# Kernel tuning notes

Hardware: AMD Instinct MI355X
Metric: run time of the kernel (lower is better)

## Reference

```python
import jax, jax.numpy as jnp
import numpy as np
import math

B, H, W = 2, 64, 64
D_MODEL = 192
D_STATE = 16
EXPAND = 1
D_INNER = EXPAND * D_MODEL
DT_RANK = math.ceil(D_MODEL / 16)  # 'auto' -> 12
DT_MIN, DT_MAX, DT_FLOOR = 0.001, 0.1, 0.0001


def setup_inputs() -> dict:
    key = jax.random.key(0)
    ks = jax.random.split(key, 10)
    x = jax.random.normal(ks[0], (B, H, W, D_MODEL), jnp.float32)
    in_proj_w = jax.random.normal(ks[1], (D_INNER, D_MODEL), jnp.float32) * (D_MODEL ** -0.5)
    in_proj_b = jnp.zeros((D_INNER,), jnp.float32)
    x_proj_w = jax.random.normal(ks[2], (2 * DT_RANK + 3 * D_STATE, D_INNER), jnp.float32) * (D_INNER ** -0.5)
    dt_init_std = DT_RANK ** -0.5
    dt_projT_w = jax.random.uniform(ks[3], (D_INNER, DT_RANK), jnp.float32, -dt_init_std, dt_init_std)
    dt_projL_w = jax.random.uniform(ks[4], (D_INNER, DT_RANK), jnp.float32, -dt_init_std, dt_init_std)
    # dt bias init: inverse-softplus of dt sampled log-uniform in [dt_min, dt_max]
    dt = jnp.exp(jax.random.uniform(ks[5], (D_INNER,), jnp.float32) * (math.log(DT_MAX) - math.log(DT_MIN)) + math.log(DT_MIN))
    dt = jnp.clip(dt, DT_FLOOR, None)
    inv_dt = dt + jnp.log(-jnp.expm1(-dt))
    dt_projT_b = inv_dt
    dt_projL_b = inv_dt
    A_init = jnp.tile(jnp.arange(1, D_STATE + 1, dtype=jnp.float32), (D_INNER, 1))  # [D_INNER, N]
    AT_log = jnp.log(A_init)
    AL_log = jnp.log(A_init)
    D_skip = jnp.ones((D_INNER,), jnp.float32)
    out_proj_w = jax.random.normal(ks[6], (D_MODEL, D_INNER), jnp.float32) * (D_INNER ** -0.5)
    out_proj_b = jnp.zeros((D_MODEL,), jnp.float32)
    return {"x": x, "in_proj_w": in_proj_w, "in_proj_b": in_proj_b, "x_proj_w": x_proj_w,
            "dt_projT_w": dt_projT_w, "dt_projT_b": dt_projT_b, "dt_projL_w": dt_projL_w,
            "dt_projL_b": dt_projL_b, "AT_log": AT_log, "AL_log": AL_log, "D_skip": D_skip,
            "out_proj_w": out_proj_w, "out_proj_b": out_proj_b}


def _wavefront_ssm(u, x_proj_w, dt_projT_w, dt_projT_b, dt_projL_w, dt_projL_b, AT_log, AL_log, D_skip):
    # u: [B,H,W,D_INNER]. 2D selective scan: state at (i,j) mixes top (i-1,j) and left (i,j-1).
    R, N = DT_RANK, D_STATE
    proj = jnp.einsum('bhwd,pd->bhwp', u, x_proj_w)  # [B,H,W,2R+3N]
    dtT_r = proj[..., :R]
    dtL_r = proj[..., R:2 * R]
    B_T = proj[..., 2 * R:2 * R + N]            # [B,H,W,N]
    B_L = proj[..., 2 * R + N:2 * R + 2 * N]    # [B,H,W,N]
    C = proj[..., 2 * R + 2 * N:]               # [B,H,W,N]
    deltaT = jax.nn.softplus(jnp.einsum('bhwr,dr->bhwd', dtT_r, dt_projT_w) + dt_projT_b)  # [B,H,W,D]
    deltaL = jax.nn.softplus(jnp.einsum('bhwr,dr->bhwd', dtL_r, dt_projL_w) + dt_projL_b)
    AT = -jnp.exp(AT_log)  # [D,N]
    AL = -jnp.exp(AL_log)
    dAT = jnp.exp(deltaT[..., None] * AT)  # [B,H,W,D,N]
    dAL = jnp.exp(deltaL[..., None] * AL)
    dB = (deltaT[..., None] * B_T[..., None, :] + deltaL[..., None] * B_L[..., None, :]) * u[..., None]  # [B,H,W,D,N]
    # reorder to [H,W,B,D,N] for scanning
    dAT_s = jnp.transpose(dAT, (1, 2, 0, 3, 4))
    dAL_s = jnp.transpose(dAL, (1, 2, 0, 3, 4))
    dB_s = jnp.transpose(dB, (1, 2, 0, 3, 4))

    def row_step(h_prev_row, row):  # h_prev_row: [W,B,D,N]
        dAT_r, dAL_r, dB_r = row
        top = dAT_r * h_prev_row + dB_r  # top-neighbor contribution + input, per column

        def col_step(h_left, cols):  # h_left: [B,D,N]
            t, a = cols
            h = t + a * h_left
            return h, h

        h0 = jnp.zeros_like(h_prev_row[0])
        _, h_row = jax.lax.scan(col_step, h0, (top, dAL_r))  # [W,B,D,N]
        return h_row, h_row

    h_init = jnp.zeros((W, u.shape[0], D_INNER, N), u.dtype)
    _, hs = jax.lax.scan(row_step, h_init, (dAT_s, dAL_s, dB_s))  # [H,W,B,D,N]
    h = jnp.transpose(hs, (2, 0, 1, 3, 4))  # [B,H,W,D,N]
    y = jnp.einsum('bhwdn,bhwn->bhwd', h, C) + u * D_skip
    return y


def reference(x, in_proj_w, in_proj_b, x_proj_w, dt_projT_w, dt_projT_b,
              dt_projL_w, dt_projL_b, AT_log, AL_log, D_skip, out_proj_w, out_proj_b):
    u = jax.nn.gelu(jnp.einsum('bhwc,dc->bhwd', x, in_proj_w) + in_proj_b, approximate=False)
    y = _wavefront_ssm(u, x_proj_w, dt_projT_w, dt_projT_b, dt_projL_w, dt_projL_b, AT_log, AL_log, D_skip)
    y = jax.nn.gelu(y, approximate=False)
    out = jnp.einsum('bhwd,cd->bhwc', y, out_proj_w) + out_proj_b
    return out
```

## Files before the change

### kernel.cpp

```cpp
#include <hip/hip_runtime.h>
#include <math.h>

#define DM 192
#define RNK 12
#define NS 16
#define NO2 432

#define OFF_FLAG   156672u
#define OFF_PY0    156688u
#define OFF_PY1    1729552u
#define OFF_YG     3302416u
#define OFF_DIAG   5268496u
#define OFF_TL2    6841360u
#define OFF_BC4D   9987088u

typedef __attribute__((ext_vector_type(8))) short short8v;
typedef __attribute__((ext_vector_type(4))) float floatx4;

__device__ __forceinline__ float gelu_f(float x){
    return 0.5f * x * (1.0f + erff(x * 0.70710678118654752f));
}
__device__ __forceinline__ float softplus_f(float x){
    return fmaxf(x, 0.0f) + log1pf(__expf(-fabsf(x)));
}
__device__ __forceinline__ int diag_off(int s){
    return (s <= 64) ? ((s * (s + 1)) >> 1) : (2080 + (((s - 64) * (191 - s)) >> 1));
}
__device__ __forceinline__ void inv_diag(int q, int& i_out, int& j_out){
    int s;
    if (q < 2080){
        s = (int)((sqrtf(8.0f * (float)q + 1.0f) - 1.0f) * 0.5f);
        while (((s + 1) * (s + 2)) / 2 <= q) s++;
        while ((s * (s + 1)) / 2 > q) s--;
    } else {
        const int q2 = 4095 - q;
        int t = (int)((sqrtf(8.0f * (float)q2 + 1.0f) - 1.0f) * 0.5f);
        while (((t + 1) * (t + 2)) / 2 <= q2) t++;
        while ((t * (t + 1)) / 2 > q2) t--;
        s = 126 - t;
    }
    const int jmin = (s > 63) ? (s - 63) : 0;
    const int j = jmin + (q - diag_off(s));
    j_out = j;
    i_out = s - j;
}
__device__ __forceinline__ unsigned short bf16_rte(float f){
    unsigned u = __float_as_uint(f);
    unsigned r = (u + 0x7fffu + ((u >> 16) & 1u)) >> 16;
    return (unsigned short)r;
}
__device__ __forceinline__ float bf16_f(unsigned short h){
    return __uint_as_float(((unsigned)h) << 16);
}
__device__ __forceinline__ void split8(float4 v0, float4 v1, short8v& hi, short8v& lo){
    float f[8] = {v0.x, v0.y, v0.z, v0.w, v1.x, v1.y, v1.z, v1.w};
    #pragma unroll
    for (int e = 0; e < 8; e++){
        unsigned short h = bf16_rte(f[e]);
        hi[e] = (short)h;
        lo[e] = (short)bf16_rte(f[e] - bf16_f(h));
    }
}

#define SW_WINH 0u
#define SW_WINL 36864u
#define SW_WCH  73728u
#define SW_WCL  156672u
#define SW_WOH  239616u
#define SW_WOL  276480u

__global__ __launch_bounds__(256) void prep_k(const float* __restrict__ Win,
                                              const float* __restrict__ xpw,
                                              const float* __restrict__ dtwT,
                                              const float* __restrict__ dtwL,
                                              const float* __restrict__ Wout,
                                              const float* __restrict__ ATl,
                                              const float* __restrict__ ALl,
                                              float* __restrict__ ws){
    unsigned short* __restrict__ wsu = (unsigned short*)ws;
    if (blockIdx.x == 612){
        __shared__ int okf;
        if (threadIdx.x == 0) okf = 1;
        __syncthreads();
        bool ok = true;
        for (int t = threadIdx.x; t < 6144; t += 256){
            const float* arr = (t < 3072) ? ATl : ALl;
            int e = (t < 3072) ? t : t - 3072;
            int n = e & 15;
            ok = ok && (fabsf(arr[e] - logf((float)(n + 1))) < 1e-5f);
        }
        if (!ok) atomicAnd(&okf, 0);
        __syncthreads();
        if (threadIdx.x == 0) ws[OFF_FLAG] = okf ? 1.0f : 0.0f;
        return;
    }
    int idx = blockIdx.x * 256 + threadIdx.x;
    float w;
    unsigned hioff, looff, rel;
    if (idx < 36864){
        w = Win[idx]; hioff = SW_WINH; looff = SW_WINL; rel = idx;
    } else if (idx < 119808){
        int t = idx - 36864;
        int o = t / DM, c = t - o * DM;
        float acc = 0.f;
        if (o < 192){
            #pragma unroll
            for (int r = 0; r < RNK; r++) acc += dtwT[o * RNK + r] * xpw[r * DM + c];
        } else if (o < 384){
            int d2 = o - 192;
            #pragma unroll
            for (int r = 0; r < RNK; r++) acc += dtwL[d2 * RNK + r] * xpw[(RNK + r) * DM + c];
        } else {
            acc = xpw[(2 * RNK + (o - 384)) * DM + c];
        }
        w = acc; hioff = SW_WCH; looff = SW_WCL; rel = t;
    } else if (idx < 156672){
        int t = idx - 119808;
        w = Wout[t]; hioff = SW_WOH; looff = SW_WOL; rel = t;
    } else return;
    unsigned short h = bf16_rte(w);
    wsu[hioff + rel] = h;
    wsu[looff + rel] = bf16_rte(w - bf16_f(h));
}

__global__ __launch_bounds__(256) void proj_k(const float* __restrict__ x,
                                              const float* __restrict__ inb,
                                              const float* __restrict__ dtTb,
                                              const float* __restrict__ dtLb,
                                              float* __restrict__ ws){
    __shared__ float u_t[16][196];
    __shared__ float g2[16][436];
    const unsigned short* __restrict__ wsu = (const unsigned short*)ws;
    const int bx = blockIdx.x;
    const int b = bx >> 8;
    const int Q0 = (bx & 255) * 16;
    const int tid = threadIdx.x;
    const int wv = tid >> 6, lane = tid & 63;
    const int lr = lane & 15, lg = lane >> 4;

    int ic, jc;
    inv_diag(Q0 + lr, ic, jc);
    const size_t xrow = ((size_t)(b << 12) + (size_t)(ic * 64 + jc)) * 192;

    short8v xh[6], xl[6];
    #pragma unroll
    for (int ks = 0; ks < 6; ks++){
        const float* xp = x + xrow + ks * 32 + lg * 8;
        split8(*(const float4*)xp, *(const float4*)(xp + 4), xh[ks], xl[ks]);
    }
    {
        floatx4 ac0 = {0.f,0.f,0.f,0.f}, ac1 = {0.f,0.f,0.f,0.f}, ac2 = {0.f,0.f,0.f,0.f};
        const int n0 = wv * 48;
        #pragma unroll
        for (int ks = 0; ks < 6; ks++){
            const size_t rb = (size_t)(n0 + lr) * 192 + ks * 32 + lg * 8;
            const short8v bh0 = *(const short8v*)(wsu + SW_WINH + rb);
            const short8v bl0 = *(const short8v*)(wsu + SW_WINL + rb);
            const short8v bh1 = *(const short8v*)(wsu + SW_WINH + rb + 16*192);
            const short8v bl1 = *(const short8v*)(wsu + SW_WINL + rb + 16*192);
            const short8v bh2 = *(const short8v*)(wsu + SW_WINH + rb + 32*192);
            const short8v bl2 = *(const short8v*)(wsu + SW_WINL + rb + 32*192);
            ac0 = __builtin_amdgcn_mfma_f32_16x16x32_bf16(xh[ks], bh0, ac0, 0, 0, 0);
            ac1 = __builtin_amdgcn_mfma_f32_16x16x32_bf16(xh[ks], bh1, ac1, 0, 0, 0);
            ac2 = __builtin_amdgcn_mfma_f32_16x16x32_bf16(xh[ks], bh2, ac2, 0, 0, 0);
            ac0 = __builtin_amdgcn_mfma_f32_16x16x32_bf16(xh[ks], bl0, ac0, 0, 0, 0);
            ac1 = __builtin_amdgcn_mfma_f32_16x16x32_bf16(xh[ks], bl1, ac1, 0, 0, 0);
            ac2 = __builtin_amdgcn_mfma_f32_16x16x32_bf16(xh[ks], bl2, ac2, 0, 0, 0);
            ac0 = __builtin_amdgcn_mfma_f32_16x16x32_bf16(xl[ks], bh0, ac0, 0, 0, 0);
            ac1 = __builtin_amdgcn_mfma_f32_16x16x32_bf16(xl[ks], bh1, ac1, 0, 0, 0);
            ac2 = __builtin_amdgcn_mfma_f32_16x16x32_bf16(xl[ks], bh2, ac2, 0, 0, 0);
        }
        const float b0 = inb[n0 + lr], b1 = inb[n0 + 16 + lr], b2 = inb[n0 + 32 + lr];
        #pragma unroll
        for (int r = 0; r < 4; r++){
            const int pl = lg * 4 + r;
            u_t[pl][n0 + lr]      = gelu_f(ac0[r] + b0);
            u_t[pl][n0 + 16 + lr] = gelu_f(ac1[r] + b1);
            u_t[pl][n0 + 32 + lr] = gelu_f(ac2[r] + b2);
        }
    }
    __syncthreads();

    {
        float* __restrict__ u_dg = ws + OFF_DIAG;
        #pragma unroll
        for (int pass = 0; pass < 3; pass++){
            const int plane = pass * 64 + (tid >> 2);
            const int posq = (tid & 3) * 4;
            float4 v = make_float4(u_t[posq + 0][plane], u_t[posq + 1][plane],
                                   u_t[posq + 2][plane], u_t[posq + 3][plane]);
            *(float4*)&u_dg[(size_t)(b * 192 + plane) * 4096 + Q0 + posq] = v;
        }
    }

    short8v uh[6], ul[6];
    #pragma unroll
    for (int ks = 0; ks < 6; ks++){
        const float* up = &u_t[lr][ks * 32 + lg * 8];
        split8(*(const float4*)up, *(const float4*)(up + 4), uh[ks], ul[ks]);
    }
    const int t0 = wv * 7;
    const int cnt = (wv == 3) ? 6 : 7;
    for (int tp = 0; tp < cnt; tp += 2){
        const bool dual = (tp + 1 < cnt);
        const int n0a = (t0 + tp) * 16, n0b = dual ? (t0 + tp + 1) * 16 : n0a;
        floatx4 acA = {0.f,0.f,0.f,0.f}, acB = {0.f,0.f,0.f,0.f};
        #pragma unroll
        for (int ks = 0; ks < 6; ks++){
            const size_t ra = (size_t)(n0a + lr) * 192 + ks * 32 + lg * 8;
            const short8v bhA = *(const short8v*)(wsu + SW_WCH + ra);
            const short8v blA = *(const short8v*)(wsu + SW_WCL + ra);
            acA = __builtin_amdgcn_mfma_f32_16x16x32_bf16(uh[ks], bhA, acA, 0, 0, 0);
            acA = __builtin_amdgcn_mfma_f32_16x16x32_bf16(uh[ks], blA, acA, 0, 0, 0);
            acA = __builtin_amdgcn_mfma_f32_16x16x32_bf16(ul[ks], bhA, acA, 0, 0, 0);
            if (dual){
                const size_t rbb = (size_t)(n0b + lr) * 192 + ks * 32 + lg * 8;
                const short8v bhB = *(const short8v*)(wsu + SW_WCH + rbb);
                const short8v blB = *(const short8v*)(wsu + SW_WCL + rbb);
                acB = __builtin_amdgcn_mfma_f32_16x16x32_bf16(uh[ks], bhB, acB, 0, 0, 0);
                acB = __builtin_amdgcn_mfma_f32_16x16x32_bf16(uh[ks], blB, acB, 0, 0, 0);
                acB = __builtin_amdgcn_mfma_f32_16x16x32_bf16(ul[ks], bhB, acB, 0, 0, 0);
            }
        }
        #pragma unroll
        for (int half = 0; half < 2; half++){
            if (half == 1 && !dual) break;
            const floatx4 ac = half ? acB : acA;
            const int o = (half ? n0b : n0a) + lr;
            float bb = 0.f; int mode = 2;
            if (o < 192){ bb = dtTb[o]; mode = 0; }
            else if (o < 384){ bb = dtLb[o - 192]; mode = 1; }
            #pragma unroll
            for (int r = 0; r < 4; r++){
                float v = ac[r];
                if (mode < 2) v = softplus_f(v + bb);
                g2[lg * 4 + r][o] = v;
            }
        }
    }
    __syncthreads();

    {
        float* __restrict__ tl_dg = ws + OFF_TL2;
        const int plane = tid >> 2;
        const int posq = (tid & 3) * 4;
        #pragma unroll
        for (int pass = 0; pass < 3; pass++){
            const int o = pass * 64 + plane;
            float4 w0 = make_float4(g2[posq + 0][o], g2[posq + 0][192 + o],
                                    g2[posq + 1][o], g2[posq + 1][192 + o]);
            float4 w1 = make_float4(g2[posq + 2][o], g2[posq + 2][192 + o],
                                    g2[posq + 3][o], g2[posq + 3][192 + o]);
            float* base = &tl_dg[(size_t)(b * 192 + o) * 8192 + (size_t)(Q0 + posq) * 2];
            *(float4*)&base[0] = w0;
            *(float4*)&base[4] = w1;
        }
        if (tid < 192){
            const int pl = tid >> 4;
            const int pos = tid & 15;
            float4 v = *(float4*)&g2[pos][384 + pl * 4];
            float4* dst = (float4*)(ws + OFF_BC4D) + (size_t)(b * 12 + pl) * 4096 + Q0 + pos;
            *dst = v;
        }
    }
}

#define LOADSET(pfx, sv) do {                                                   \
    const int sc_ = (sv) < 126 ? (sv) : 126;                                    \
    const int jmin_ = (sc_ > 63) ? (sc_ - 63) : 0;                              \
    pfx##_q = diag_off(sc_) - jmin_ + j;                                        \
    pfx##_u = pu[pfx##_q];                                                      \
    pfx##_tv = ptl[pfx##_q];                                                    \
    pfx##_bt = pBT[pfx##_q]; pfx##_bl = pBL[pfx##_q]; pfx##_cc = pC[pfx##_q];   \
} while (0)

#define STEP(pfx, sv) do {                                                      \
    const float dT_ = pfx##_tv.x, dL_ = pfx##_tv.y, u_ = pfx##_u;               \
    const float bt_[4] = {pfx##_bt.x, pfx##_bt.y, pfx##_bt.z, pfx##_bt.w};      \
    const float bl_[4] = {pfx##_bl.x, pfx##_bl.y, pfx##_bl.z, pfx##_bl.w};      \
    const float cc_[4] = {pfx##_cc.x, pfx##_cc.y, pfx##_cc.z, pfx##_cc.w};      \
    const int q_ = pfx##_q;                                                     \
    LOADSET(pfx, (sv) + 5);                                                     \
    float da_[4], dl_[4];                                                       \
    if (sflag){                                                                 \
        const float E_ = __expf(-dT_), F_ = __expf(-dL_);                       \
        da_[0] = __expf(nA1 * dT_); dl_[0] = __expf(nA1 * dL_);                 \
        da_[1] = da_[0] * E_; da_[2] = da_[1] * E_; da_[3] = da_[2] * E_;       \
        dl_[1] = dl_[0] * F_; dl_[2] = dl_[1] * F_; dl_[3] = dl_[2] * F_;       \
    } else {                                                                    \
        da_[0] = __expf(dT_ * ATr[0]); da_[1] = __expf(dT_ * ATr[1]);           \
        da_[2] = __expf(dT_ * ATr[2]); da_[3] = __expf(dT_ * ATr[3]);           \
        dl_[0] = __expf(dL_ * ALr[0]); dl_[1] = __expf(dL_ * ALr[1]);           \
        dl_[2] = __expf(dL_ * ALr[2]); dl_[3] = __expf(dL_ * ALr[3]);           \
    }                                                                           \
    const int ic_ = (sv) - j;                                                   \
    const bool act_ = ((unsigned)ic_) < 64u;                                    \
    const float udT_ = u_ * dT_, udL_ = u_ * dL_;                               \
    float y_ = 0.f;                                                             \
    _Pragma("unroll")                                                           \
    for (int k = 0; k < 4; k++){                                                \
        float hl_ = __shfl_up(h[k], 1u, 64);                                    \
        hl_ = (j == 0) ? 0.f : hl_;                                             \
        float hn_ = fmaf(da_[k], h[k], fmaf(dl_[k], hl_, fmaf(udT_, bt_[k], udL_ * bl_[k]))); \
        h[k] = act_ ? hn_ : h[k];                                               \
        y_ = fmaf(hn_, cc_[k], y_);                                             \
    }                                                                           \
    if (act_) ylds[wv][q_] = y_;                                                \
} while (0)

__global__ __launch_bounds__(128) void scan_k(const float* __restrict__ ATl,
                                              const float* __restrict__ ALl,
                                              float* __restrict__ ws){
    __shared__ float ylds[2][4096];
    const int bx = blockIdx.x;
    const int half = (bx >= 384) ? 1 : 0;
    const int bd = bx - half * 384;
    const int b = bd / 192, d = bd - b * 192;
    const int tid = threadIdx.x;
    const int wv = tid >> 6, j = tid & 63;
    const int n0 = half * 8 + wv * 4;
    const int ng = half * 2 + wv;

    const float* __restrict__ pu = ws + OFF_DIAG + (size_t)bd * 4096;
    const float2* __restrict__ ptl = (const float2*)(ws + OFF_TL2 + (size_t)bd * 8192);
    const float4* __restrict__ bc4 = (const float4*)(ws + OFF_BC4D) + (size_t)(b * 12) * 4096;
    const float4* __restrict__ pBT = bc4 + (size_t)(0 + ng) * 4096;
    const float4* __restrict__ pBL = bc4 + (size_t)(4 + ng) * 4096;
    const float4* __restrict__ pC  = bc4 + (size_t)(8 + ng) * 4096;
    float* __restrict__ pY = ws + (half ? OFF_PY1 : OFF_PY0) + (size_t)bd * 4096;

    const bool sflag = (ws[OFF_FLAG] > 0.5f);
    const float nA1 = -(float)(n0 + 1);
    float ATr[4], ALr[4];
    if (!sflag){
        #pragma unroll
        for (int k = 0; k < 4; k++){
            ATr[k] = -expf(ATl[d * NS + n0 + k]);
            ALr[k] = -expf(ALl[d * NS + n0 + k]);
        }
    } else {
        #pragma unroll
        for (int k = 0; k < 4; k++){ ATr[k] = 0.f; ALr[k] = 0.f; }
    }
    float h[4] = {0.f, 0.f, 0.f, 0.f};

    int a_q, b_q, c_q, d_q, e_q;
    float a_u; float2 a_tv; float4 a_bt, a_bl, a_cc;
    float b_u; float2 b_tv; float4 b_bt, b_bl, b_cc;
    float c_u; float2 c_tv; float4 c_bt, c_bl, c_cc;
    float d_u; float2 d_tv; float4 d_bt, d_bl, d_cc;
    float e_u; float2 e_tv; float4 e_bt, e_bl, e_cc;
    LOADSET(a, 0);
    LOADSET(b, 1);
    LOADSET(c, 2);
    LOADSET(d, 3);
    LOADSET(e, 4);

    for (int s = 0; s < 130; s += 5){
        STEP(a, s);
        STEP(b, s + 1);
        STEP(c, s + 2);
        STEP(d, s + 3);
        STEP(e, s + 4);
    }

    __syncthreads();
    for (int idx = tid; idx < 4096; idx += 128)
        pY[idx] = ylds[0][idx] + ylds[1][idx];
}

__global__ __launch_bounds__(256) void ysum_k(const float* __restrict__ Dskp,
                                              float* __restrict__ ws){
    __shared__ float yl[4096];
    const int bd = blockIdx.x;
    const int d = bd % 192;
    const int tid = threadIdx.x;
    const float* __restrict__ p0 = ws + OFF_PY0 + (size_t)bd * 4096;
    const float* __restrict__ p1 = ws + OFF_PY1 + (size_t)bd * 4096;
    const float* __restrict__ pu = ws + OFF_DIAG + (size_t)bd * 4096;
    float* __restrict__ yg = ws + OFF_YG + (size_t)bd * 4096;
    const float Dsk = Dskp[d];
    #pragma unroll
    for (int k = 0; k < 16; k++){
        const int idx = tid + k * 256;
        yl[idx] = gelu_f(p0[idx] + p1[idx] + pu[idx] * Dsk);
    }
    __syncthreads();
    #pragma unroll
    for (int k = 0; k < 16; k++){
        const int idx = tid + k * 256;
        const int i = idx >> 6, jj = idx & 63;
        const int s = i + jj;
        const int jmin = (s > 63) ? (s - 63) : 0;
        yg[idx] = yl[diag_off(s) + jj - jmin];
    }
}

__global__ __launch_bounds__(256) void out_k(const float* __restrict__ Wob,
                                             float* __restrict__ ws,
                                             float* __restrict__ out){
    __shared__ float yg_t[16][196];
    const unsigned short* __restrict__ wsu = (const unsigned short*)ws;
    const int P0 = blockIdx.x * 16;
    const int b = P0 >> 12;
    const int prel = P0 & 4095;
    const int tid = threadIdx.x;

    {
        const float* __restrict__ ygp = ws + OFF_YG;
        #pragma unroll
        for (int pass = 0; pass < 3; pass++){
            const int plane = pass * 64 + (tid >> 2);
            const int posq = (tid & 3) * 4;
            float4 v = *(const float4*)&ygp[(size_t)(b * 192 + plane) * 4096 + prel + posq];
            yg_t[posq + 0][plane] = v.x;
            yg_t[posq + 1][plane] = v.y;
            yg_t[posq + 2][plane] = v.z;
            yg_t[posq + 3][plane] = v.w;
        }
    }
    __syncthreads();

    const int wv = tid >> 6, lane = tid & 63;
    const int lr = lane & 15, lg = lane >> 4;

    short8v yh[6], yl2[6];
    #pragma unroll
    for (int ks = 0; ks < 6; ks++){
        const float* yp = &yg_t[lr][ks * 32 + lg * 8];
        split8(*(const float4*)yp, *(const float4*)(yp + 4), yh[ks], yl2[ks]);
    }
    {
        floatx4 ac0 = {0.f,0.f,0.f,0.f}, ac1 = {0.f,0.f,0.f,0.f}, ac2 = {0.f,0.f,0.f,0.f};
        const int n0 = wv * 48;
        #pragma unroll
        for (int ks = 0; ks < 6; ks++){
            const size_t rb = (size_t)(n0 + lr) * 192 + ks * 32 + lg * 8;
            const short8v bh0 = *(const short8v*)(wsu + SW_WOH + rb);
            const short8v bl0 = *(const short8v*)(wsu + SW_WOL + rb);
            const short8v bh1 = *(const short8v*)(wsu + SW_WOH + rb + 16*192);
            const short8v bl1 = *(const short8v*)(wsu + SW_WOL + rb + 16*192);
            const short8v bh2 = *(const short8v*)(wsu + SW_WOH + rb + 32*192);
            const short8v bl2 = *(const short8v*)(wsu + SW_WOL + rb + 32*192);
            ac0 = __builtin_amdgcn_mfma_f32_16x16x32_bf16(yh[ks], bh0, ac0, 0, 0, 0);
            ac1 = __builtin_amdgcn_mfma_f32_16x16x32_bf16(yh[ks], bh1, ac1, 0, 0, 0);
            ac2 = __builtin_amdgcn_mfma_f32_16x16x32_bf16(yh[ks], bh2, ac2, 0, 0, 0);
            ac0 = __builtin_amdgcn_mfma_f32_16x16x32_bf16(yh[ks], bl0, ac0, 0, 0, 0);
            ac1 = __builtin_amdgcn_mfma_f32_16x16x32_bf16(yh[ks], bl1, ac1, 0, 0, 0);
            ac2 = __builtin_amdgcn_mfma_f32_16x16x32_bf16(yh[ks], bl2, ac2, 0, 0, 0);
            ac0 = __builtin_amdgcn_mfma_f32_16x16x32_bf16(yl2[ks], bh0, ac0, 0, 0, 0);
            ac1 = __builtin_amdgcn_mfma_f32_16x16x32_bf16(yl2[ks], bh1, ac1, 0, 0, 0);
            ac2 = __builtin_amdgcn_mfma_f32_16x16x32_bf16(yl2[ks], bh2, ac2, 0, 0, 0);
        }
        const float b0 = Wob[n0 + lr], b1 = Wob[n0 + 16 + lr], b2 = Wob[n0 + 32 + lr];
        #pragma unroll
        for (int r = 0; r < 4; r++){
            const int pos = P0 + lg * 4 + r;
            out[(size_t)pos * 192 + n0 + lr]      = ac0[r] + b0;
            out[(size_t)pos * 192 + n0 + 16 + lr] = ac1[r] + b1;
            out[(size_t)pos * 192 + n0 + 32 + lr] = ac2[r] + b2;
        }
    }
}

extern "C" void kernel_launch(void* const* d_in, const int* in_sizes, int n_in,
                              void* d_out, int out_size, void* d_ws, size_t ws_size,
                              hipStream_t stream) {
    const float* x    = (const float*)d_in[0];
    const float* Win  = (const float*)d_in[1];
    const float* Winb = (const float*)d_in[2];
    const float* xpw  = (const float*)d_in[3];
    const float* dtTw = (const float*)d_in[4];
    const float* dtTb = (const float*)d_in[5];
    const float* dtLw = (const float*)d_in[6];
    const float* dtLb = (const float*)d_in[7];
    const float* ATl  = (const float*)d_in[8];
    const float* ALl  = (const float*)d_in[9];
    const float* Dsk  = (const float*)d_in[10];
    const float* Wo   = (const float*)d_in[11];
    const float* Wob  = (const float*)d_in[12];
    float* out = (float*)d_out;
    float* ws  = (float*)d_ws;

    hipLaunchKernelGGL(prep_k,   dim3(613), dim3(256), 0, stream, Win, xpw, dtTw, dtLw, Wo, ATl, ALl, ws);
    hipLaunchKernelGGL(proj_k,   dim3(512), dim3(256), 0, stream, x, Winb, dtTb, dtLb, ws);
    hipLaunchKernelGGL(scan_k,   dim3(768), dim3(128), 0, stream, ATl, ALl, ws);
    hipLaunchKernelGGL(ysum_k,   dim3(384), dim3(256), 0, stream, Dsk, ws);
    hipLaunchKernelGGL(out_k,    dim3(512), dim3(256), 0, stream, Wob, ws, out);
}
```

Baseline: 121.0 us.

## Store B/C scan coefficients as bf16 and deepen scan prefetch to six steps

The B_T, B_L and C coefficients consumed by the wavefront scan are now packed as bf16 pairs (uint2 instead of float4), halving their memory traffic per step. The software pipeline in scan_k is deepened from 5 to 6 outstanding load sets, and launch bounds request two blocks per SM. This trades numeric precision of B/C (bf16 rounding) for bandwidth and latency hiding, and adds a few extra steps of loop overrun with more live registers.

```diff
diff --git a/kernel.cpp b/kernel.cpp
--- a/kernel.cpp
+++ b/kernel.cpp
@@ -12,7 +12,7 @@
 #define OFF_YG     3302416u
 #define OFF_DIAG   5268496u
 #define OFF_TL2    6841360u
-#define OFF_BC4D   9987088u
+#define OFF_BC16   9987088u
 
 typedef __attribute__((ext_vector_type(8))) short short8v;
 typedef __attribute__((ext_vector_type(4))) float floatx4;
@@ -52,6 +52,11 @@
 __device__ __forceinline__ float bf16_f(unsigned short h){
     return __uint_as_float(((unsigned)h) << 16);
 }
+__device__ __forceinline__ unsigned pack2bf(float lo, float hi){
+    return (unsigned)bf16_rte(lo) | ((unsigned)bf16_rte(hi) << 16);
+}
+__device__ __forceinline__ float bl2f(unsigned v){ return __uint_as_float(v << 16); }
+__device__ __forceinline__ float bh2f(unsigned v){ return __uint_as_float(v & 0xffff0000u); }
 __device__ __forceinline__ void split8(float4 v0, float4 v1, short8v& hi, short8v& lo){
     float f[8] = {v0.x, v0.y, v0.z, v0.w, v1.x, v1.y, v1.z, v1.w};
     #pragma unroll
@@ -258,8 +263,12 @@
         if (tid < 192){
             const int pl = tid >> 4;
             const int pos = tid & 15;
-            float4 v = *(float4*)&g2[pos][384 + pl * 4];
-            float4* dst = (float4*)(ws + OFF_BC4D) + (size_t)(b * 12 + pl) * 4096 + Q0 + pos;
+            const float s0 = g2[pos][384 + pl * 4 + 0];
+            const float s1 = g2[pos][384 + pl * 4 + 1];
+            const float s2 = g2[pos][384 + pl * 4 + 2];
+            const float s3 = g2[pos][384 + pl * 4 + 3];
+            uint2 v = make_uint2(pack2bf(s0, s1), pack2bf(s2, s3));
+            uint2* dst = (uint2*)(ws + OFF_BC16) + (size_t)(b * 12 + pl) * 4096 + Q0 + pos;
             *dst = v;
         }
     }
@@ -276,11 +285,14 @@
 
 #define STEP(pfx, sv) do {                                                      \
     const float dT_ = pfx##_tv.x, dL_ = pfx##_tv.y, u_ = pfx##_u;               \
-    const float bt_[4] = {pfx##_bt.x, pfx##_bt.y, pfx##_bt.z, pfx##_bt.w};      \
-    const float bl_[4] = {pfx##_bl.x, pfx##_bl.y, pfx##_bl.z, pfx##_bl.w};      \
-    const float cc_[4] = {pfx##_cc.x, pfx##_cc.y, pfx##_cc.z, pfx##_cc.w};      \
+    const float bt_[4] = {bl2f(pfx##_bt.x), bh2f(pfx##_bt.x),                   \
+                          bl2f(pfx##_bt.y), bh2f(pfx##_bt.y)};                  \
+    const float bl_[4] = {bl2f(pfx##_bl.x), bh2f(pfx##_bl.x),                   \
+                          bl2f(pfx##_bl.y), bh2f(pfx##_bl.y)};                  \
+    const float cc_[4] = {bl2f(pfx##_cc.x), bh2f(pfx##_cc.x),                   \
+                          bl2f(pfx##_cc.y), bh2f(pfx##_cc.y)};                  \
     const int q_ = pfx##_q;                                                     \
-    LOADSET(pfx, (sv) + 5);                                                     \
+    LOADSET(pfx, (sv) + 6);                                                     \
     float da_[4], dl_[4];                                                       \
     if (sflag){                                                                 \
         const float E_ = __expf(-dT_), F_ = __expf(-dL_);                       \
@@ -308,9 +320,9 @@
     if (act_) ylds[wv][q_] = y_;                                                \
 } while (0)
 
-__global__ __launch_bounds__(128) void scan_k(const float* __restrict__ ATl,
-                                              const float* __restrict__ ALl,
-                                              float* __restrict__ ws){
+__global__ __launch_bounds__(128, 2) void scan_k(const float* __restrict__ ATl,
+                                                 const float* __restrict__ ALl,
+                                                 float* __restrict__ ws){
     __shared__ float ylds[2][4096];
     const int bx = blockIdx.x;
     const int half = (bx >= 384) ? 1 : 0;
@@ -323,10 +335,10 @@
 
     const float* __restrict__ pu = ws + OFF_DIAG + (size_t)bd * 4096;
     const float2* __restrict__ ptl = (const float2*)(ws + OFF_TL2 + (size_t)bd * 8192);
-    const float4* __restrict__ bc4 = (const float4*)(ws + OFF_BC4D) + (size_t)(b * 12) * 4096;
-    const float4* __restrict__ pBT = bc4 + (size_t)(0 + ng) * 4096;
-    const float4* __restrict__ pBL = bc4 + (size_t)(4 + ng) * 4096;
-    const float4* __restrict__ pC  = bc4 + (size_t)(8 + ng) * 4096;
+    const uint2* __restrict__ bc16 = (const uint2*)(ws + OFF_BC16) + (size_t)(b * 12) * 4096;
+    const uint2* __restrict__ pBT = bc16 + (size_t)(0 + ng) * 4096;
+    const uint2* __restrict__ pBL = bc16 + (size_t)(4 + ng) * 4096;
+    const uint2* __restrict__ pC  = bc16 + (size_t)(8 + ng) * 4096;
     float* __restrict__ pY = ws + (half ? OFF_PY1 : OFF_PY0) + (size_t)bd * 4096;
 
     const bool sflag = (ws[OFF_FLAG] > 0.5f);
@@ -344,24 +356,27 @@
     }
     float h[4] = {0.f, 0.f, 0.f, 0.f};
 
-    int a_q, b_q, c_q, d_q, e_q;
-    float a_u; float2 a_tv; float4 a_bt, a_bl, a_cc;
-    float b_u; float2 b_tv; float4 b_bt, b_bl, b_cc;
-    float c_u; float2 c_tv; float4 c_bt, c_bl, c_cc;
-    float d_u; float2 d_tv; float4 d_bt, d_bl, d_cc;
-    float e_u; float2 e_tv; float4 e_bt, e_bl, e_cc;
+    int a_q, b_q, c_q, d_q, e_q, f_q;
+    float a_u; float2 a_tv; uint2 a_bt, a_bl, a_cc;
+    float b_u; float2 b_tv; uint2 b_bt, b_bl, b_cc;
+    float c_u; float2 c_tv; uint2 c_bt, c_bl, c_cc;
+    float d_u; float2 d_tv; uint2 d_bt, d_bl, d_cc;
+    float e_u; float2 e_tv; uint2 e_bt, e_bl, e_cc;
+    float f_u; float2 f_tv; uint2 f_bt, f_bl, f_cc;
     LOADSET(a, 0);
     LOADSET(b, 1);
     LOADSET(c, 2);
     LOADSET(d, 3);
     LOADSET(e, 4);
-
-    for (int s = 0; s < 130; s += 5){
+    LOADSET(f, 5);
+
+    for (int s = 0; s < 132; s += 6){
         STEP(a, s);
         STEP(b, s + 1);
         STEP(c, s + 2);
         STEP(d, s + 3);
         STEP(e, s + 4);
+        STEP(f, s + 5);
     }
 
     __syncthreads();
```

New measurement: 124.3 us. 2.7% more time.

## Split scan state across four waves per block with bf16 partial-y staging

Applied to the files above, without the earlier changes.

The scan kernel now runs 256 threads per block, with each wave owning 2 state channels instead of 4, so twice as many waves share the wavefront recurrence. Each step does less serial work and needs fewer registers. The prefetch depth drops from 5 to 3 steps, and B/C vectors are loaded as float2 slices of the existing float4 layout. Per-wave partial y values are stored in LDS as bf16 to fit four copies, which loses precision in the summed output. The change relies on bf16 helper functions defined elsewhere in the file.

```diff
diff --git a/kernel.cpp b/kernel.cpp
--- a/kernel.cpp
+++ b/kernel.cpp
@@ -271,102 +271,94 @@
     pfx##_q = diag_off(sc_) - jmin_ + j;                                        \
     pfx##_u = pu[pfx##_q];                                                      \
     pfx##_tv = ptl[pfx##_q];                                                    \
-    pfx##_bt = pBT[pfx##_q]; pfx##_bl = pBL[pfx##_q]; pfx##_cc = pC[pfx##_q];   \
+    pfx##_bt = *(const float2*)(pBT + 4 * pfx##_q);                             \
+    pfx##_bl = *(const float2*)(pBL + 4 * pfx##_q);                             \
+    pfx##_cc = *(const float2*)(pC  + 4 * pfx##_q);                             \
 } while (0)
 
 #define STEP(pfx, sv) do {                                                      \
     const float dT_ = pfx##_tv.x, dL_ = pfx##_tv.y, u_ = pfx##_u;               \
-    const float bt_[4] = {pfx##_bt.x, pfx##_bt.y, pfx##_bt.z, pfx##_bt.w};      \
-    const float bl_[4] = {pfx##_bl.x, pfx##_bl.y, pfx##_bl.z, pfx##_bl.w};      \
-    const float cc_[4] = {pfx##_cc.x, pfx##_cc.y, pfx##_cc.z, pfx##_cc.w};      \
+    const float bt0_ = pfx##_bt.x, bt1_ = pfx##_bt.y;                           \
+    const float bl0_ = pfx##_bl.x, bl1_ = pfx##_bl.y;                           \
+    const float cc0_ = pfx##_cc.x, cc1_ = pfx##_cc.y;                           \
     const int q_ = pfx##_q;                                                     \
-    LOADSET(pfx, (sv) + 5);                                                     \
-    float da_[4], dl_[4];                                                       \
+    LOADSET(pfx, (sv) + 3);                                                     \
+    float da0_, da1_, dl0_, dl1_;                                               \
     if (sflag){                                                                 \
-        const float E_ = __expf(-dT_), F_ = __expf(-dL_);                       \
-        da_[0] = __expf(nA1 * dT_); dl_[0] = __expf(nA1 * dL_);                 \
-        da_[1] = da_[0] * E_; da_[2] = da_[1] * E_; da_[3] = da_[2] * E_;       \
-        dl_[1] = dl_[0] * F_; dl_[2] = dl_[1] * F_; dl_[3] = dl_[2] * F_;       \
+        da0_ = __expf(nA1 * dT_); da1_ = da0_ * __expf(-dT_);                   \
+        dl0_ = __expf(nA1 * dL_); dl1_ = dl0_ * __expf(-dL_);                   \
     } else {                                                                    \
-        da_[0] = __expf(dT_ * ATr[0]); da_[1] = __expf(dT_ * ATr[1]);           \
-        da_[2] = __expf(dT_ * ATr[2]); da_[3] = __expf(dT_ * ATr[3]);           \
-        dl_[0] = __expf(dL_ * ALr[0]); dl_[1] = __expf(dL_ * ALr[1]);           \
-        dl_[2] = __expf(dL_ * ALr[2]); dl_[3] = __expf(dL_ * ALr[3]);           \
+        da0_ = __expf(dT_ * ATr[0]); da1_ = __expf(dT_ * ATr[1]);               \
+        dl0_ = __expf(dL_ * ALr[0]); dl1_ = __expf(dL_ * ALr[1]);               \
     }                                                                           \
     const int ic_ = (sv) - j;                                                   \
     const bool act_ = ((unsigned)ic_) < 64u;                                    \
     const float udT_ = u_ * dT_, udL_ = u_ * dL_;                               \
     float y_ = 0.f;                                                             \
-    _Pragma("unroll")                                                           \
-    for (int k = 0; k < 4; k++){                                                \
-        float hl_ = __shfl_up(h[k], 1u, 64);                                    \
-        hl_ = (j == 0) ? 0.f : hl_;                                             \
-        float hn_ = fmaf(da_[k], h[k], fmaf(dl_[k], hl_, fmaf(udT_, bt_[k], udL_ * bl_[k]))); \
-        h[k] = act_ ? hn_ : h[k];                                               \
-        y_ = fmaf(hn_, cc_[k], y_);                                             \
-    }                                                                           \
-    if (act_) ylds[wv][q_] = y_;                                                \
+    { float hl_ = __shfl_up(h0, 1u, 64); hl_ = (j == 0) ? 0.f : hl_;            \
+      float hn_ = fmaf(da0_, h0, fmaf(dl0_, hl_, fmaf(udT_, bt0_, udL_ * bl0_))); \
+      h0 = act_ ? hn_ : h0; y_ = fmaf(hn_, cc0_, y_); }                         \
+    { float hl_ = __shfl_up(h1, 1u, 64); hl_ = (j == 0) ? 0.f : hl_;            \
+      float hn_ = fmaf(da1_, h1, fmaf(dl1_, hl_, fmaf(udT_, bt1_, udL_ * bl1_))); \
+      h1 = act_ ? hn_ : h1; y_ = fmaf(hn_, cc1_, y_); }                         \
+    if (act_) ylds[(wv << 12) + q_] = bf16_rte(y_);                             \
 } while (0)
 
-__global__ __launch_bounds__(128) void scan_k(const float* __restrict__ ATl,
+__global__ __launch_bounds__(256) void scan_k(const float* __restrict__ ATl,
                                               const float* __restrict__ ALl,
                                               float* __restrict__ ws){
-    __shared__ float ylds[2][4096];
+    __shared__ unsigned short ylds[4 * 4096];
     const int bx = blockIdx.x;
     const int half = (bx >= 384) ? 1 : 0;
     const int bd = bx - half * 384;
     const int b = bd / 192, d = bd - b * 192;
     const int tid = threadIdx.x;
     const int wv = tid >> 6, j = tid & 63;
-    const int n0 = half * 8 + wv * 4;
-    const int ng = half * 2 + wv;
+    const int n0 = half * 8 + wv * 2;
+    const int g4 = n0 >> 2;
+    const int hw = wv & 1;
 
     const float* __restrict__ pu = ws + OFF_DIAG + (size_t)bd * 4096;
     const float2* __restrict__ ptl = (const float2*)(ws + OFF_TL2 + (size_t)bd * 8192);
-    const float4* __restrict__ bc4 = (const float4*)(ws + OFF_BC4D) + (size_t)(b * 12) * 4096;
-    const float4* __restrict__ pBT = bc4 + (size_t)(0 + ng) * 4096;
-    const float4* __restrict__ pBL = bc4 + (size_t)(4 + ng) * 4096;
-    const float4* __restrict__ pC  = bc4 + (size_t)(8 + ng) * 4096;
+    const float* __restrict__ bcb = ws + OFF_BC4D + (size_t)(b * 12) * 16384;
+    const float* __restrict__ pBT = bcb + (size_t)(0 + g4) * 16384 + hw * 2;
+    const float* __restrict__ pBL = bcb + (size_t)(4 + g4) * 16384 + hw * 2;
+    const float* __restrict__ pC  = bcb + (size_t)(8 + g4) * 16384 + hw * 2;
     float* __restrict__ pY = ws + (half ? OFF_PY1 : OFF_PY0) + (size_t)bd * 4096;
 
     const bool sflag = (ws[OFF_FLAG] > 0.5f);
     const float nA1 = -(float)(n0 + 1);
-    float ATr[4], ALr[4];
+    float ATr[2], ALr[2];
     if (!sflag){
         #pragma unroll
-        for (int k = 0; k < 4; k++){
+        for (int k = 0; k < 2; k++){
             ATr[k] = -expf(ATl[d * NS + n0 + k]);
             ALr[k] = -expf(ALl[d * NS + n0 + k]);
         }
     } else {
-        #pragma unroll
-        for (int k = 0; k < 4; k++){ ATr[k] = 0.f; ALr[k] = 0.f; }
-    }
-    float h[4] = {0.f, 0.f, 0.f, 0.f};
-
-    int a_q, b_q, c_q, d_q, e_q;
-    float a_u; float2 a_tv; float4 a_bt, a_bl, a_cc;
-    float b_u; float2 b_tv; float4 b_bt, b_bl, b_cc;
-    float c_u; float2 c_tv; float4 c_bt, c_bl, c_cc;
-    float d_u; float2 d_tv; float4 d_bt, d_bl, d_cc;
-    float e_u; float2 e_tv; float4 e_bt, e_bl, e_cc;
+        ATr[0] = ATr[1] = ALr[0] = ALr[1] = 0.f;
+    }
+    float h0 = 0.f, h1 = 0.f;
+
+    int a_q, b_q, c_q;
+    float a_u; float2 a_tv, a_bt, a_bl, a_cc;
+    float b_u; float2 b_tv, b_bt, b_bl, b_cc;
+    float c_u; float2 c_tv, c_bt, c_bl, c_cc;
     LOADSET(a, 0);
     LOADSET(b, 1);
     LOADSET(c, 2);
-    LOADSET(d, 3);
-    LOADSET(e, 4);
-
-    for (int s = 0; s < 130; s += 5){
+
+    for (int s = 0; s < 129; s += 3){
         STEP(a, s);
         STEP(b, s + 1);
         STEP(c, s + 2);
-        STEP(d, s + 3);
-        STEP(e, s + 4);
     }
 
     __syncthreads();
-    for (int idx = tid; idx < 4096; idx += 128)
-        pY[idx] = ylds[0][idx] + ylds[1][idx];
+    for (int idx = tid; idx < 4096; idx += 256){
+        pY[idx] = bf16_f(ylds[idx]) + bf16_f(ylds[4096 + idx]) +
+                  bf16_f(ylds[8192 + idx]) + bf16_f(ylds[12288 + idx]);
+    }
 }
 
 __global__ __launch_bounds__(256) void ysum_k(const float* __restrict__ Dskp,
@@ -484,7 +476,7 @@
 
     hipLaunchKernelGGL(prep_k,   dim3(613), dim3(256), 0, stream, Win, xpw, dtTw, dtLw, Wo, ATl, ALl, ws);
     hipLaunchKernelGGL(proj_k,   dim3(512), dim3(256), 0, stream, x, Winb, dtTb, dtLb, ws);
-    hipLaunchKernelGGL(scan_k,   dim3(768), dim3(128), 0, stream, ATl, ALl, ws);
+    hipLaunchKernelGGL(scan_k,   dim3(768), dim3(256), 0, stream, ATl, ALl, ws);
     hipLaunchKernelGGL(ysum_k,   dim3(384), dim3(256), 0, stream, Dsk, ws);
     hipLaunchKernelGGL(out_k,    dim3(512), dim3(256), 0, stream, Wob, ws, out);
 }
```

New measurement: 134.6 us. 1.11x slower.

## Fuse ysum into scan kernel with 4-wave blocks covering all states

Applied to the files above, without the earlier changes.

The scan kernel now uses 256-thread blocks, with four waves covering all 16 states of a (batch, channel) pair, instead of two blocks of two waves each. This lets the partial-y reduction, the D-skip term, GELU and the diagonal-to-grid reorder run in the same kernel through 64KB of LDS. The two partial-y global buffers and the separate ysum launch go away. It also drops the prefetch depth from 5 to 4 diagonals. The trade is half as many blocks and higher LDS use per block, which may reduce occupancy and latency hiding in the serial scan.

```diff
diff --git a/kernel.cpp b/kernel.cpp
--- a/kernel.cpp
+++ b/kernel.cpp
@@ -280,7 +280,7 @@
     const float bl_[4] = {pfx##_bl.x, pfx##_bl.y, pfx##_bl.z, pfx##_bl.w};      \
     const float cc_[4] = {pfx##_cc.x, pfx##_cc.y, pfx##_cc.z, pfx##_cc.w};      \
     const int q_ = pfx##_q;                                                     \
-    LOADSET(pfx, (sv) + 5);                                                     \
+    LOADSET(pfx, (sv) + 4);                                                     \
     float da_[4], dl_[4];                                                       \
     if (sflag){                                                                 \
         const float E_ = __expf(-dT_), F_ = __expf(-dL_);                       \
@@ -305,21 +305,20 @@
         h[k] = act_ ? hn_ : h[k];                                               \
         y_ = fmaf(hn_, cc_[k], y_);                                             \
     }                                                                           \
-    if (act_) ylds[wv][q_] = y_;                                                \
+    if (act_) ylds[(wv << 12) + q_] = y_;                                       \
 } while (0)
 
-__global__ __launch_bounds__(128) void scan_k(const float* __restrict__ ATl,
+__global__ __launch_bounds__(256) void scan_k(const float* __restrict__ ATl,
                                               const float* __restrict__ ALl,
+                                              const float* __restrict__ Dskp,
                                               float* __restrict__ ws){
-    __shared__ float ylds[2][4096];
-    const int bx = blockIdx.x;
-    const int half = (bx >= 384) ? 1 : 0;
-    const int bd = bx - half * 384;
+    __shared__ float ylds[4 * 4096];
+    const int bd = blockIdx.x;
     const int b = bd / 192, d = bd - b * 192;
     const int tid = threadIdx.x;
     const int wv = tid >> 6, j = tid & 63;
-    const int n0 = half * 8 + wv * 4;
-    const int ng = half * 2 + wv;
+    const int n0 = wv * 4;
+    const int ng = wv;
 
     const float* __restrict__ pu = ws + OFF_DIAG + (size_t)bd * 4096;
     const float2* __restrict__ ptl = (const float2*)(ws + OFF_TL2 + (size_t)bd * 8192);
@@ -327,7 +326,6 @@
     const float4* __restrict__ pBT = bc4 + (size_t)(0 + ng) * 4096;
     const float4* __restrict__ pBL = bc4 + (size_t)(4 + ng) * 4096;
     const float4* __restrict__ pC  = bc4 + (size_t)(8 + ng) * 4096;
-    float* __restrict__ pY = ws + (half ? OFF_PY1 : OFF_PY0) + (size_t)bd * 4096;
 
     const bool sflag = (ws[OFF_FLAG] > 0.5f);
     const float nA1 = -(float)(n0 + 1);
@@ -344,55 +342,37 @@
     }
     float h[4] = {0.f, 0.f, 0.f, 0.f};
 
-    int a_q, b_q, c_q, d_q, e_q;
+    int a_q, b_q, c_q, d_q;
     float a_u; float2 a_tv; float4 a_bt, a_bl, a_cc;
     float b_u; float2 b_tv; float4 b_bt, b_bl, b_cc;
     float c_u; float2 c_tv; float4 c_bt, c_bl, c_cc;
     float d_u; float2 d_tv; float4 d_bt, d_bl, d_cc;
-    float e_u; float2 e_tv; float4 e_bt, e_bl, e_cc;
     LOADSET(a, 0);
     LOADSET(b, 1);
     LOADSET(c, 2);
     LOADSET(d, 3);
-    LOADSET(e, 4);
-
-    for (int s = 0; s < 130; s += 5){
+
+    for (int s = 0; s < 128; s += 4){
         STEP(a, s);
         STEP(b, s + 1);
         STEP(c, s + 2);
         STEP(d, s + 3);
-        STEP(e, s + 4);
     }
 
     __syncthreads();
-    for (int idx = tid; idx < 4096; idx += 128)
-        pY[idx] = ylds[0][idx] + ylds[1][idx];
-}
-
-__global__ __launch_bounds__(256) void ysum_k(const float* __restrict__ Dskp,
-                                              float* __restrict__ ws){
-    __shared__ float yl[4096];
-    const int bd = blockIdx.x;
-    const int d = bd % 192;
-    const int tid = threadIdx.x;
-    const float* __restrict__ p0 = ws + OFF_PY0 + (size_t)bd * 4096;
-    const float* __restrict__ p1 = ws + OFF_PY1 + (size_t)bd * 4096;
-    const float* __restrict__ pu = ws + OFF_DIAG + (size_t)bd * 4096;
+    const float Dsk = Dskp[d];
+    for (int idx = tid; idx < 4096; idx += 256){
+        const float v = ylds[idx] + ylds[4096 + idx] + ylds[8192 + idx] + ylds[12288 + idx]
+                      + pu[idx] * Dsk;
+        ylds[idx] = gelu_f(v);
+    }
+    __syncthreads();
     float* __restrict__ yg = ws + OFF_YG + (size_t)bd * 4096;
-    const float Dsk = Dskp[d];
-    #pragma unroll
-    for (int k = 0; k < 16; k++){
-        const int idx = tid + k * 256;
-        yl[idx] = gelu_f(p0[idx] + p1[idx] + pu[idx] * Dsk);
-    }
-    __syncthreads();
-    #pragma unroll
-    for (int k = 0; k < 16; k++){
-        const int idx = tid + k * 256;
+    for (int idx = tid; idx < 4096; idx += 256){
         const int i = idx >> 6, jj = idx & 63;
         const int s = i + jj;
         const int jmin = (s > 63) ? (s - 63) : 0;
-        yg[idx] = yl[diag_off(s) + jj - jmin];
+        yg[idx] = ylds[diag_off(s) + jj - jmin];
     }
 }
 
@@ -484,7 +464,6 @@
 
     hipLaunchKernelGGL(prep_k,   dim3(613), dim3(256), 0, stream, Win, xpw, dtTw, dtLw, Wo, ATl, ALl, ws);
     hipLaunchKernelGGL(proj_k,   dim3(512), dim3(256), 0, stream, x, Winb, dtTb, dtLb, ws);
-    hipLaunchKernelGGL(scan_k,   dim3(768), dim3(128), 0, stream, ATl, ALl, ws);
-    hipLaunchKernelGGL(ysum_k,   dim3(384), dim3(256), 0, stream, Dsk, ws);
+    hipLaunchKernelGGL(scan_k,   dim3(384), dim3(256), 0, stream, ATl, ALl, Dsk, ws);
     hipLaunchKernelGGL(out_k,    dim3(512), dim3(256), 0, stream, Wob, ws, out);
 }
```

Result: faster. 113.5 us (-6.2%).
